# Optimization experiments

Measured on AMD Instinct MI355X. Metric: run time of the kernel, lower is better.

The kernel has to match this reference:

```python
import jax, jax.numpy as jnp
import numpy as np

NUM_PROJS = 7
BLOCK = 32

def _gray_perm(n):
    # unit-hamming-distance (Gray-code) permutation used by AngularLSH
    a = np.array([0, 1], dtype=np.int32)
    for s in range(2, n + 1):
        a = np.concatenate([a, a[::-1] + 2 ** (s - 1)])
    return a

PERM = jnp.asarray(_gray_perm(NUM_PROJS))
ENC = jnp.asarray(2 ** np.arange(NUM_PROJS), dtype=np.int32)  # [R]


def lsh_hash(x, proj_dir):
    # x: [B,H,S,D], proj_dir: [D,R] -> integer bucket ids [B,H,S]
    bits = (jnp.einsum('bhsd,dr->bhsr', x, proj_dir) > 0).astype(jnp.int32)
    code = (bits * ENC).sum(-1)
    return PERM[code]


def sdpa(q, k, v, mask):
    # q,k,v: [...,S,D]; mask: bool broadcastable to [...,Sq,Sk]
    scale = q.shape[-1] ** -0.5
    scores = jnp.einsum('...qd,...kd->...qk', q, k) * scale
    scores = jnp.where(mask, scores, -jnp.inf)
    return jnp.einsum('...qk,...kd->...qd', jax.nn.softmax(scores, axis=-1), v)


def setup_inputs() -> dict:
    key = jax.random.key(0)
    kq, kk, kv, kp = jax.random.split(key, 4)
    B, H, S, D = 2, 16, 2048, 128
    return {
        'q': jax.random.normal(kq, (B, H, S, D), dtype=jnp.float32),
        'k': jax.random.normal(kk, (B, H, S, D), dtype=jnp.float32),
        'v': jax.random.normal(kv, (B, H, S, D), dtype=jnp.float32),
        'proj_dir': jax.random.normal(kp, (D, NUM_PROJS), dtype=jnp.float32),
        'mask': jnp.ones((1, 1, 1, 1), dtype=bool),
    }


def reference(q, k, v, proj_dir, mask):
    B, H, S, D = q.shape
    # 1) LSH hash queries, stable sort along seq dim, reorder queries
    q_hash = lsh_hash(q, proj_dir)                                   # [B,H,S]
    sort_idx = jnp.argsort(q_hash, axis=2, stable=True)              # [B,H,S]
    q_hash_sorted = jnp.take_along_axis(q_hash, sort_idx, axis=2)
    q_sorted = jnp.take_along_axis(q, sort_idx[..., None], axis=2)   # [B,H,S,D]
    # 2) hash keys (unsorted), split into blocks of size BLOCK
    k_hash = lsh_hash(k, proj_dir)                                   # [B,H,S]
    k_hash_blk = k_hash.reshape(-1, 1, BLOCK)                        # [NB,1,32]
    q_hash_blk = q_hash_sorted.reshape(-1, 1, BLOCK)
    # 3) criticality: per-block count of matching hash ids; critical blocks get K zeroed
    criticality = (k_hash_blk == q_hash_blk).sum(-1).squeeze(-1)     # [NB]
    keep = (criticality <= 0).astype(q.dtype)                        # 0 where critical (matches torch loop)
    Qb = q_sorted.reshape(-1, 1, BLOCK, D)                           # [NB,1,32,D]
    Kb = k.reshape(-1, 1, BLOCK, D) * keep[:, None, None, None]
    Vb = v.reshape(-1, 1, BLOCK, D)
    # 4) dual SDPA: blocked critical attention + full dense attention
    out_critical = sdpa(Qb, Kb, Vb, mask).reshape(B, H, S, D)
    out_actual = sdpa(q, k, v, mask)                                 # [B,H,S,D]
    loss = jnp.mean((out_critical - out_actual) ** 2)
    return out_actual, loss
```

## Files before the change

kernel.cpp:

```cpp
#include <hip/hip_runtime.h>
#include <hip/hip_bf16.h>

#define SEQ 2048
#define DIM 128
#define NBH 32
#define NROWS (NBH*SEQ)
#define NBLK (NROWS/32)
#define SCALE 0.08838834764831845f
#define QSC (0.08838834764831845f * 1.4426950408889634f)

typedef __attribute__((ext_vector_type(8))) short short8;
typedef __attribute__((ext_vector_type(16))) float float16;

__device__ __forceinline__ unsigned short f2bf(float x) {
    union { float f; unsigned u; } v; v.f = x;
    unsigned r = v.u + 0x7fffu + ((v.u >> 16) & 1u);
    return (unsigned short)(r >> 16);
}
__device__ __forceinline__ unsigned pack_bf16(float a, float b) {
    float2 f; f.x = a; f.y = b;
    __hip_bfloat162 h = __float22bfloat162_rn(f);
    union { __hip_bfloat162 h2; unsigned u; } cv; cv.h2 = h; return cv.u;
}
__device__ __forceinline__ void gl_lds16(const void* g, void* l) {
    __builtin_amdgcn_global_load_lds((const __attribute__((address_space(1))) unsigned int*)g,
                                     (__attribute__((address_space(3))) unsigned int*)l, 16, 0, 0);
}

__global__ __launch_bounds__(256) void hash_kernel(const float* __restrict__ qg, const float* __restrict__ kg,
                            const float* __restrict__ proj,
                            int* __restrict__ qh, int* __restrict__ kh)
{
    const int gw   = (int)((blockIdx.x * blockDim.x + threadIdx.x) >> 6);
    const int lane = threadIdx.x & 63;
    const int sub  = lane >> 4;
    const int dl   = (lane & 15) * 8;
    const int r    = gw * 4 + sub;
    const float* src; int* dst; int row;
    if (r < NROWS) { src = qg; dst = qh; row = r; }
    else           { src = kg; dst = kh; row = r - NROWS; }

    const float* x = src + (size_t)row * DIM + dl;
    float xv[8];
    {
        float4 f0 = *(const float4*)x;
        float4 f1 = *(const float4*)(x + 4);
        xv[0]=f0.x; xv[1]=f0.y; xv[2]=f0.z; xv[3]=f0.w;
        xv[4]=f1.x; xv[5]=f1.y; xv[6]=f1.z; xv[7]=f1.w;
    }
    float pj[56];
    #pragma unroll
    for (int i = 0; i < 14; ++i)
        *(float4*)&pj[i*4] = *(const float4*)(proj + dl*7 + i*4);

    float a[7] = {0.f,0.f,0.f,0.f,0.f,0.f,0.f};
    #pragma unroll
    for (int d = 0; d < 8; ++d)
        #pragma unroll
        for (int p = 0; p < 7; ++p) a[p] = fmaf(xv[d], pj[d*7+p], a[p]);

    #pragma unroll
    for (int off = 1; off < 16; off <<= 1)
        #pragma unroll
        for (int p = 0; p < 7; ++p) a[p] += __shfl_xor(a[p], off, 64);

    if ((lane & 15) == 0) {
        int code = 0;
        if (a[0] > 0.f) code |= 1;  if (a[1] > 0.f) code |= 2;
        if (a[2] > 0.f) code |= 4;  if (a[3] > 0.f) code |= 8;
        if (a[4] > 0.f) code |= 16; if (a[5] > 0.f) code |= 32;
        if (a[6] > 0.f) code |= 64;
        dst[row] = code ^ (code >> 1);
    }
}

__global__ __launch_bounds__(256) void sort_kernel(const int* __restrict__ qh,
                                                   int* __restrict__ sidx, int* __restrict__ qhs)
{
    __shared__ unsigned short cnt[128][260];
    __shared__ int startv[128];
    const int bh = blockIdx.x;
    const int t  = threadIdx.x;
    const int base = bh*SEQ;

    for (int i = t; i < 128*260; i += 256) ((unsigned short*)cnt)[i] = 0;
    __syncthreads();

    int hv[8];
    {
        int4 a = *(const int4*)(qh + base + t*8);
        int4 b = *(const int4*)(qh + base + t*8 + 4);
        hv[0]=a.x; hv[1]=a.y; hv[2]=a.z; hv[3]=a.w;
        hv[4]=b.x; hv[5]=b.y; hv[6]=b.z; hv[7]=b.w;
    }
    #pragma unroll
    for (int i = 0; i < 8; ++i) cnt[hv[i]][t]++;
    __syncthreads();

    const int wv = t >> 6, l = t & 63;
    #pragma unroll 1
    for (int v = wv; v < 128; v += 4) {
        ushort4 cc = *(const ushort4*)&cnt[v][4*l];
        unsigned c0 = cc.x, c1 = cc.y, c2 = cc.z, c3 = cc.w;
        unsigned s01 = c0 + c1;
        unsigned s = s01 + c2 + c3;
        unsigned inc = s;
        #pragma unroll
        for (int off = 1; off < 64; off <<= 1) {
            unsigned o = __shfl_up(inc, off, 64);
            if (l >= off) inc += o;
        }
        unsigned ex = inc - s;
        ushort4 wb;
        wb.x = (unsigned short)ex;
        wb.y = (unsigned short)(ex + c0);
        wb.z = (unsigned short)(ex + s01);
        wb.w = (unsigned short)(ex + s01 + c2);
        *(ushort4*)&cnt[v][4*l] = wb;
        if (l == 63) cnt[v][256] = (unsigned short)inc;
    }
    __syncthreads();

    if (t < 64) {
        int a0 = cnt[2*t][256], a1 = cnt[2*t+1][256];
        int s2 = a0 + a1, inc = s2;
        #pragma unroll
        for (int off = 1; off < 64; off <<= 1) {
            int o = __shfl_up(inc, off, 64);
            if (t >= off) inc += o;
        }
        int ex = inc - s2;
        startv[2*t]   = ex;
        startv[2*t+1] = ex + a0;
    }
    __syncthreads();

    #pragma unroll
    for (int i = 0; i < 8; ++i) {
        const int v = hv[i];
        int prior = 0;
        #pragma unroll
        for (int j = 0; j < 8; ++j) if (j < i && hv[j] == v) ++prior;
        const int rank = startv[v] + (int)cnt[v][t] + prior;
        sidx[base + rank] = t*8 + i;
        qhs[base + rank]  = v;
    }
}

__global__ void crit_kernel(const int* __restrict__ kh, const int* __restrict__ qhs,
                            float* __restrict__ keepg)
{
    int nb = blockIdx.x * blockDim.x + threadIdx.x;
    if (nb >= NBLK) return;
    int c = 0;
    #pragma unroll
    for (int i = 0; i < 32; ++i) c += (kh[nb*32+i] == qhs[nb*32+i]) ? 1 : 0;
    keepg[nb] = (c == 0) ? 1.0f : 0.0f;
}

__global__ __launch_bounds__(256) void prep_kernel(const float* __restrict__ kg,
                                                   const float* __restrict__ vg,
                                                   unsigned short* __restrict__ kbf,
                                                   unsigned short* __restrict__ vtg)
{
    __shared__ unsigned short T[128][72];
    const int t  = threadIdx.x;
    const int h  = blockIdx.x >> 5;
    const int sl = blockIdx.x & 31;
    const size_t base = ((size_t)h*SEQ + sl*64) * DIM;

    #pragma unroll
    for (int i = 0; i < 8; ++i) {
        const float4 f = *(const float4*)(kg + base + ((size_t)i*256 + t)*4);
        uint2 pk; pk.x = pack_bf16(f.x, f.y); pk.y = pack_bf16(f.z, f.w);
        *(uint2*)(kbf + base + ((size_t)i*256 + t)*4) = pk;
    }

    const int kk = t & 63, seg = t >> 6;
    #pragma unroll
    for (int i = 0; i < 8; ++i) {
        float4 f = *(const float4*)(vg + base + (size_t)kk*DIM + seg*32 + i*4);
        T[seg*32 + i*4 + 0][kk] = f2bf(f.x);
        T[seg*32 + i*4 + 1][kk] = f2bf(f.y);
        T[seg*32 + i*4 + 2][kk] = f2bf(f.z);
        T[seg*32 + i*4 + 3][kk] = f2bf(f.w);
    }
    __syncthreads();
    const int r = t >> 1, hf = t & 1;
    unsigned short* dst = vtg + ((size_t)h*DIM + r)*SEQ + sl*64 + hf*32;
    #pragma unroll
    for (int i = 0; i < 4; ++i)
        *(short8*)(dst + i*8) = *(const short8*)&T[r][hf*32 + i*8];
}

__global__ __launch_bounds__(256, 2) void dense_attn_mfma(
    const unsigned short* __restrict__ kbf, const unsigned short* __restrict__ vtg,
    const float* __restrict__ qg, float* __restrict__ outg)
{
    __shared__ __align__(16) unsigned short KbF[2*8192];
    __shared__ __align__(16) unsigned short VbF[2*8192];

    const int t    = threadIdx.x;
    const int lane = t & 63;
    const int w    = t >> 6;
    const int q5   = lane >> 5;
    const int l31  = lane & 31;
    const int e    = l31 & 7;

    const int b    = blockIdx.x;
    const int slot = b >> 3;
    const int head = (b & 7) * 4 + (slot >> 4);
    const int qblk = slot & 15;

    const float* Qg = qg + ((size_t)head*SEQ + qblk*128 + w*32) * DIM;
    const unsigned short* Kh = kbf + (size_t)head*SEQ*DIM;
    const unsigned short* Vh = vtg + (size_t)head*DIM*SEQ;

    int koff[8], voff[4];
    #pragma unroll
    for (int ch = 0; ch < 8; ++ch) koff[ch] = l31*128 + (((2*ch + q5) ^ e) * 8);
    #pragma unroll
    for (int u = 0; u < 4; ++u)    voff[u]  = l31*64  + ((((u>>1)*4 + (u&1)*2 + q5) ^ e) * 8);

    const unsigned short* kgp[4]; unsigned short* kls[4];
    const unsigned short* vgp[4]; unsigned short* vls[4];
    #pragma unroll
    for (int i = 0; i < 4; ++i) {
        const int j = w*4 + i;
        const int r = j*4 + (lane >> 4);
        const int u = (lane & 15) ^ (r & 7);
        kgp[i] = Kh + r*DIM + u*8;
        kls[i] = KbF + j*512;
        const int d = j*8 + (lane >> 3);
        const int u2 = (lane & 7) ^ (d & 7);
        vgp[i] = Vh + (size_t)d*SEQ + u2*8;
        vls[i] = VbF + j*512;
    }

    union FR { unsigned u[4]; short8 s; };
    short8 Qf[8];
    #pragma unroll
    for (int ch = 0; ch < 8; ++ch) {
        const float* p = Qg + (size_t)l31*DIM + ch*16 + q5*8;
        float4 f0 = *(const float4*)p;
        float4 f1 = *(const float4*)(p + 4);
        FR fr;
        fr.u[0] = pack_bf16(f0.x*QSC, f0.y*QSC);
        fr.u[1] = pack_bf16(f0.z*QSC, f0.w*QSC);
        fr.u[2] = pack_bf16(f1.x*QSC, f1.y*QSC);
        fr.u[3] = pack_bf16(f1.z*QSC, f1.w*QSC);
        Qf[ch] = fr.s;
    }

    float16 o[4];
    #pragma unroll
    for (int mt = 0; mt < 4; ++mt)
        #pragma unroll
        for (int r = 0; r < 16; ++r) o[mt][r] = 0.f;
    float lsum = 0.f;

    auto stage = [&](const int buf) {
        #pragma unroll
        for (int i = 0; i < 4; ++i) gl_lds16(kgp[i], kls[i] + buf*8192);
        #pragma unroll
        for (int i = 0; i < 4; ++i) gl_lds16(vgp[i], vls[i] + buf*8192);
        #pragma unroll
        for (int i = 0; i < 4; ++i) { kgp[i] += 8192; vgp[i] += 64; }
    };

    auto body = [&](const int buf) {
        #pragma unroll
        for (int s = 0; s < 2; ++s) {
            float16 sv;
            #pragma unroll
            for (int r = 0; r < 16; ++r) sv[r] = 0.f;
            __builtin_amdgcn_s_setprio(1);
            #pragma unroll
            for (int ch = 0; ch < 8; ++ch) {
                short8 kf = *(const short8*)&KbF[buf*8192 + s*4096 + koff[ch]];
                sv = __builtin_amdgcn_mfma_f32_32x32x16_bf16(kf, Qf[ch], sv, 0, 0, 0);
            }
            __builtin_amdgcn_s_setprio(0);
            unsigned pk[8];
            #pragma unroll
            for (int rp = 0; rp < 8; ++rp) {
                float p0 = __builtin_amdgcn_exp2f(sv[2*rp]);
                float p1 = __builtin_amdgcn_exp2f(sv[2*rp+1]);
                lsum += p0 + p1;
                pk[rp] = pack_bf16(p0, p1);
            }
            unsigned e0 = __shfl_xor(q5 ? pk[0] : pk[2], 32, 64);
            unsigned e1 = __shfl_xor(q5 ? pk[1] : pk[3], 32, 64);
            unsigned e2 = __shfl_xor(q5 ? pk[4] : pk[6], 32, 64);
            unsigned e3 = __shfl_xor(q5 ? pk[5] : pk[7], 32, 64);
            FR c0, c1;
            if (q5 == 0) {
                c0.u[0]=pk[0]; c0.u[1]=pk[1]; c0.u[2]=e0;    c0.u[3]=e1;
                c1.u[0]=pk[4]; c1.u[1]=pk[5]; c1.u[2]=e2;    c1.u[3]=e3;
            } else {
                c0.u[0]=e0;    c0.u[1]=e1;    c0.u[2]=pk[2]; c0.u[3]=pk[3];
                c1.u[0]=e2;    c1.u[1]=e3;    c1.u[2]=pk[6]; c1.u[3]=pk[7];
            }
            __builtin_amdgcn_s_setprio(1);
            #pragma unroll
            for (int c = 0; c < 2; ++c) {
                short8 pf = c ? c1.s : c0.s;
                #pragma unroll
                for (int mt = 0; mt < 4; ++mt) {
                    short8 vf = *(const short8*)&VbF[buf*8192 + mt*2048 + voff[s*2 + c]];
                    o[mt] = __builtin_amdgcn_mfma_f32_32x32x16_bf16(vf, pf, o[mt], 0, 0, 0);
                }
            }
            __builtin_amdgcn_s_setprio(0);
        }
    };

    stage(0);
    stage(1);
    #pragma unroll 1
    for (int kt2 = 0; kt2 < 15; ++kt2) {
        asm volatile("s_waitcnt vmcnt(8)" ::: "memory");
        __builtin_amdgcn_s_barrier();
        body(0);
        asm volatile("s_waitcnt lgkmcnt(0)" ::: "memory");
        __builtin_amdgcn_s_barrier();
        stage(0);
        asm volatile("s_waitcnt vmcnt(8)" ::: "memory");
        __builtin_amdgcn_s_barrier();
        body(1);
        asm volatile("s_waitcnt lgkmcnt(0)" ::: "memory");
        __builtin_amdgcn_s_barrier();
        stage(1);
    }
    asm volatile("s_waitcnt vmcnt(8)" ::: "memory");
    __builtin_amdgcn_s_barrier();
    body(0);
    asm volatile("s_waitcnt vmcnt(0)" ::: "memory");
    __builtin_amdgcn_s_barrier();
    body(1);

    const float l = lsum + __shfl_xor(lsum, 32, 64);
    const float inv = 1.f / l;
    float* orow = outg + ((size_t)head*SEQ + qblk*128 + w*32 + l31) * DIM;
    #pragma unroll
    for (int mt = 0; mt < 4; ++mt)
        #pragma unroll
        for (int rg = 0; rg < 4; ++rg) {
            const int d0 = mt*32 + rg*8 + q5*4;
            float4 ov;
            ov.x = o[mt][rg*4+0]*inv; ov.y = o[mt][rg*4+1]*inv;
            ov.z = o[mt][rg*4+2]*inv; ov.w = o[mt][rg*4+3]*inv;
            *(float4*)(orow + d0) = ov;
        }
}

__global__ __launch_bounds__(256) void crit_attn(
    const unsigned short* __restrict__ kbf, const unsigned short* __restrict__ vtg,
    const float* __restrict__ qg, const int* __restrict__ sidx,
    const float* __restrict__ keepg, const float* __restrict__ outg, float* __restrict__ lossp)
{
    __shared__ float wsum[4];
    const int t    = threadIdx.x;
    const int lane = t & 63;
    const int w    = t >> 6;
    const int nb   = blockIdx.x * 4 + w;
    const int q5   = lane >> 5;
    const int l31  = lane & 31;
    const int bh   = nb >> 6;

    const float kp = keepg[nb];
    const int qrow = sidx[bh*SEQ + (nb & 63)*32 + l31];

    union FR { unsigned u[4]; short8 s; };
    short8 Qf[8];
    const float* Qg = qg + ((size_t)bh*SEQ + qrow) * DIM;
    #pragma unroll
    for (int ch = 0; ch < 8; ++ch) {
        const float* p = Qg + ch*16 + q5*8;
        float4 f0 = *(const float4*)p;
        float4 f1 = *(const float4*)(p + 4);
        FR fr;
        fr.u[0] = pack_bf16(f0.x*QSC, f0.y*QSC);
        fr.u[1] = pack_bf16(f0.z*QSC, f0.w*QSC);
        fr.u[2] = pack_bf16(f1.x*QSC, f1.y*QSC);
        fr.u[3] = pack_bf16(f1.z*QSC, f1.w*QSC);
        Qf[ch] = fr.s;
    }

    const unsigned short* Kb = kbf + (size_t)(nb*32) * DIM;
    float16 sv;
    #pragma unroll
    for (int r = 0; r < 16; ++r) sv[r] = 0.f;
    #pragma unroll
    for (int ch = 0; ch < 8; ++ch) {
        short8 kf = *(const short8*)(Kb + (size_t)l31*DIM + ch*16 + q5*8);
        sv = __builtin_amdgcn_mfma_f32_32x32x16_bf16(kf, Qf[ch], sv, 0, 0, 0);
    }

    float lsum = 0.f;
    unsigned pk[8];
    #pragma unroll
    for (int rp = 0; rp < 8; ++rp) {
        float p0 = __builtin_amdgcn_exp2f(sv[2*rp]   * kp);
        float p1 = __builtin_amdgcn_exp2f(sv[2*rp+1] * kp);
        lsum += p0 + p1;
        pk[rp] = pack_bf16(p0, p1);
    }
    unsigned e0 = __shfl_xor(q5 ? pk[0] : pk[2], 32, 64);
    unsigned e1 = __shfl_xor(q5 ? pk[1] : pk[3], 32, 64);
    unsigned e2 = __shfl_xor(q5 ? pk[4] : pk[6], 32, 64);
    unsigned e3 = __shfl_xor(q5 ? pk[5] : pk[7], 32, 64);
    FR c0, c1;
    if (q5 == 0) {
        c0.u[0]=pk[0]; c0.u[1]=pk[1]; c0.u[2]=e0;    c0.u[3]=e1;
        c1.u[0]=pk[4]; c1.u[1]=pk[5]; c1.u[2]=e2;    c1.u[3]=e3;
    } else {
        c0.u[0]=e0;    c0.u[1]=e1;    c0.u[2]=pk[2]; c0.u[3]=pk[3];
        c1.u[0]=e2;    c1.u[1]=e3;    c1.u[2]=pk[6]; c1.u[3]=pk[7];
    }
    const float ltot = lsum + __shfl_xor(lsum, 32, 64);

    const unsigned short* Vb = vtg + (size_t)bh*DIM*SEQ + (size_t)(nb & 63)*32;
    float16 o[4];
    #pragma unroll
    for (int mt = 0; mt < 4; ++mt)
        #pragma unroll
        for (int r = 0; r < 16; ++r) o[mt][r] = 0.f;
    #pragma unroll
    for (int c = 0; c < 2; ++c) {
        short8 pf = c ? c1.s : c0.s;
        #pragma unroll
        for (int mt = 0; mt < 4; ++mt) {
            short8 vf = *(const short8*)(Vb + (size_t)(mt*32 + l31)*SEQ + c*16 + q5*8);
            o[mt] = __builtin_amdgcn_mfma_f32_32x32x16_bf16(vf, pf, o[mt], 0, 0, 0);
        }
    }

    const float inv = 1.f / ltot;
    const float* oa_row = outg + (size_t)(nb*32 + l31) * DIM;
    float sq = 0.f;
    #pragma unroll
    for (int mt = 0; mt < 4; ++mt)
        #pragma unroll
        for (int rg = 0; rg < 4; ++rg) {
            const int d0 = mt*32 + rg*8 + q5*4;
            float4 oa = *(const float4*)(oa_row + d0);
            float dx = o[mt][rg*4+0]*inv - oa.x;
            float dy = o[mt][rg*4+1]*inv - oa.y;
            float dz = o[mt][rg*4+2]*inv - oa.z;
            float dw = o[mt][rg*4+3]*inv - oa.w;
            sq += dx*dx + dy*dy + dz*dz + dw*dw;
        }
    #pragma unroll
    for (int off = 32; off > 0; off >>= 1) sq += __shfl_down(sq, off, 64);
    if (lane == 0) wsum[w] = sq;
    __syncthreads();
    if (t == 0) atomicAdd(lossp, (wsum[0]+wsum[1]+wsum[2]+wsum[3]) * (1.0f/8388608.0f));
}

extern "C" void kernel_launch(void* const* d_in, const int* in_sizes, int n_in,
                              void* d_out, int out_size, void* d_ws, size_t ws_size,
                              hipStream_t stream)
{
    const float* q    = (const float*)d_in[0];
    const float* k    = (const float*)d_in[1];
    const float* v    = (const float*)d_in[2];
    const float* proj = (const float*)d_in[3];
    float* out   = (float*)d_out;
    float* lossp = out + (out_size - 1);

    int* qh   = (int*)d_ws;
    int* kh   = qh + NROWS;
    int* sidx = kh + NROWS;
    int* qhs  = sidx + NROWS;
    float* keepg = (float*)(qhs + NROWS);
    unsigned short* kbf = (unsigned short*)(keepg + NBLK);
    unsigned short* vtg = kbf + (size_t)NROWS*DIM;

    hipMemsetAsync(lossp, 0, sizeof(float), stream);
    prep_kernel<<<NBH*32, 256, 0, stream>>>(k, v, kbf, vtg);
    hash_kernel<<<(2*NROWS)/16, 256, 0, stream>>>(q, k, proj, qh, kh);
    sort_kernel<<<NBH, 256, 0, stream>>>(qh, sidx, qhs);
    crit_kernel<<<NBLK/256, 256, 0, stream>>>(kh, qhs, keepg);
    dense_attn_mfma<<<512, 256, 0, stream>>>(kbf, vtg, q, out);
    crit_attn<<<NBLK/4, 256, 0, stream>>>(kbf, vtg, q, sidx, keepg, out, lossp);
}
```

Before: 283.9 us.

## Fuse criticality into crit_attn, split QK MFMA chains, simplify dense pipeline

Removes the separate crit_kernel launch and computes each block's keep flag inside crit_attn using a wave ballot over the key and sorted query hashes. Both attention kernels now split the QK dot product into two independent MFMA accumulator chains, which shortens the dependency chain at the cost of extra registers. The dense kernel's loop is restructured into a single loop that prefetches only one tile ahead and waits on vmcnt(0) every iteration. That drops the earlier deeper prefetch, so less load latency may be hidden.

```diff
diff --git a/kernel.cpp b/kernel.cpp
--- a/kernel.cpp
+++ b/kernel.cpp
@@ -145,17 +145,6 @@
         sidx[base + rank] = t*8 + i;
         qhs[base + rank]  = v;
     }
-}
-
-__global__ void crit_kernel(const int* __restrict__ kh, const int* __restrict__ qhs,
-                            float* __restrict__ keepg)
-{
-    int nb = blockIdx.x * blockDim.x + threadIdx.x;
-    if (nb >= NBLK) return;
-    int c = 0;
-    #pragma unroll
-    for (int i = 0; i < 32; ++i) c += (kh[nb*32+i] == qhs[nb*32+i]) ? 1 : 0;
-    keepg[nb] = (c == 0) ? 1.0f : 0.0f;
 }
 
 __global__ __launch_bounds__(256) void prep_kernel(const float* __restrict__ kg,
@@ -237,6 +226,17 @@
         vls[i] = VbF + j*512;
     }
 
+    auto stage = [&](const int buf) {
+        #pragma unroll
+        for (int i = 0; i < 4; ++i) gl_lds16(kgp[i], kls[i] + buf*8192);
+        #pragma unroll
+        for (int i = 0; i < 4; ++i) gl_lds16(vgp[i], vls[i] + buf*8192);
+        #pragma unroll
+        for (int i = 0; i < 4; ++i) { kgp[i] += 8192; vgp[i] += 64; }
+    };
+
+    stage(0);
+
     union FR { unsigned u[4]; short8 s; };
     short8 Qf[8];
     #pragma unroll
@@ -257,36 +257,29 @@
     for (int mt = 0; mt < 4; ++mt)
         #pragma unroll
         for (int r = 0; r < 16; ++r) o[mt][r] = 0.f;
-    float lsum = 0.f;
-
-    auto stage = [&](const int buf) {
-        #pragma unroll
-        for (int i = 0; i < 4; ++i) gl_lds16(kgp[i], kls[i] + buf*8192);
-        #pragma unroll
-        for (int i = 0; i < 4; ++i) gl_lds16(vgp[i], vls[i] + buf*8192);
-        #pragma unroll
-        for (int i = 0; i < 4; ++i) { kgp[i] += 8192; vgp[i] += 64; }
-    };
+    float lsum0 = 0.f, lsum1 = 0.f;
 
     auto body = [&](const int buf) {
         #pragma unroll
         for (int s = 0; s < 2; ++s) {
-            float16 sv;
+            float16 sv, sw;
             #pragma unroll
-            for (int r = 0; r < 16; ++r) sv[r] = 0.f;
+            for (int r = 0; r < 16; ++r) { sv[r] = 0.f; sw[r] = 0.f; }
             __builtin_amdgcn_s_setprio(1);
             #pragma unroll
-            for (int ch = 0; ch < 8; ++ch) {
+            for (int ch = 0; ch < 4; ++ch) {
                 short8 kf = *(const short8*)&KbF[buf*8192 + s*4096 + koff[ch]];
                 sv = __builtin_amdgcn_mfma_f32_32x32x16_bf16(kf, Qf[ch], sv, 0, 0, 0);
+                short8 kg2 = *(const short8*)&KbF[buf*8192 + s*4096 + koff[ch+4]];
+                sw = __builtin_amdgcn_mfma_f32_32x32x16_bf16(kg2, Qf[ch+4], sw, 0, 0, 0);
             }
             __builtin_amdgcn_s_setprio(0);
             unsigned pk[8];
             #pragma unroll
             for (int rp = 0; rp < 8; ++rp) {
-                float p0 = __builtin_amdgcn_exp2f(sv[2*rp]);
-                float p1 = __builtin_amdgcn_exp2f(sv[2*rp+1]);
-                lsum += p0 + p1;
+                float p0 = __builtin_amdgcn_exp2f(sv[2*rp]   + sw[2*rp]);
+                float p1 = __builtin_amdgcn_exp2f(sv[2*rp+1] + sw[2*rp+1]);
+                lsum0 += p0; lsum1 += p1;
                 pk[rp] = pack_bf16(p0, p1);
             }
             unsigned e0 = __shfl_xor(q5 ? pk[0] : pk[2], 32, 64);
@@ -315,30 +308,15 @@
         }
     };
 
-    stage(0);
-    stage(1);
-    #pragma unroll 1
-    for (int kt2 = 0; kt2 < 15; ++kt2) {
-        asm volatile("s_waitcnt vmcnt(8)" ::: "memory");
+    #pragma unroll 2
+    for (int kt = 0; kt < 32; ++kt) {
+        asm volatile("s_waitcnt vmcnt(0) lgkmcnt(0)" ::: "memory");
         __builtin_amdgcn_s_barrier();
-        body(0);
-        asm volatile("s_waitcnt lgkmcnt(0)" ::: "memory");
-        __builtin_amdgcn_s_barrier();
-        stage(0);
-        asm volatile("s_waitcnt vmcnt(8)" ::: "memory");
-        __builtin_amdgcn_s_barrier();
-        body(1);
-        asm volatile("s_waitcnt lgkmcnt(0)" ::: "memory");
-        __builtin_amdgcn_s_barrier();
-        stage(1);
-    }
-    asm volatile("s_waitcnt vmcnt(8)" ::: "memory");
-    __builtin_amdgcn_s_barrier();
-    body(0);
-    asm volatile("s_waitcnt vmcnt(0)" ::: "memory");
-    __builtin_amdgcn_s_barrier();
-    body(1);
-
+        if (kt < 31) stage((kt & 1) ^ 1);
+        body(kt & 1);
+    }
+
+    const float lsum = lsum0 + lsum1;
     const float l = lsum + __shfl_xor(lsum, 32, 64);
     const float inv = 1.f / l;
     float* orow = outg + ((size_t)head*SEQ + qblk*128 + w*32 + l31) * DIM;
@@ -357,7 +335,8 @@
 __global__ __launch_bounds__(256) void crit_attn(
     const unsigned short* __restrict__ kbf, const unsigned short* __restrict__ vtg,
     const float* __restrict__ qg, const int* __restrict__ sidx,
-    const float* __restrict__ keepg, const float* __restrict__ outg, float* __restrict__ lossp)
+    const int* __restrict__ kh, const int* __restrict__ qhs,
+    const float* __restrict__ outg, float* __restrict__ lossp)
 {
     __shared__ float wsum[4];
     const int t    = threadIdx.x;
@@ -368,7 +347,11 @@
     const int l31  = lane & 31;
     const int bh   = nb >> 6;
 
-    const float kp = keepg[nb];
+    const int khv = kh[nb*32 + l31];
+    const int qhv = qhs[nb*32 + l31];
+    const unsigned long long mm = __ballot(khv == qhv);
+    const float kp = ((mm & 0xffffffffull) == 0ull) ? 1.0f : 0.0f;
+
     const int qrow = sidx[bh*SEQ + (nb & 63)*32 + l31];
 
     union FR { unsigned u[4]; short8 s; };
@@ -388,21 +371,23 @@
     }
 
     const unsigned short* Kb = kbf + (size_t)(nb*32) * DIM;
-    float16 sv;
-    #pragma unroll
-    for (int r = 0; r < 16; ++r) sv[r] = 0.f;
-    #pragma unroll
-    for (int ch = 0; ch < 8; ++ch) {
+    float16 sv, sw;
+    #pragma unroll
+    for (int r = 0; r < 16; ++r) { sv[r] = 0.f; sw[r] = 0.f; }
+    #pragma unroll
+    for (int ch = 0; ch < 4; ++ch) {
         short8 kf = *(const short8*)(Kb + (size_t)l31*DIM + ch*16 + q5*8);
         sv = __builtin_amdgcn_mfma_f32_32x32x16_bf16(kf, Qf[ch], sv, 0, 0, 0);
+        short8 kg2 = *(const short8*)(Kb + (size_t)l31*DIM + (ch+4)*16 + q5*8);
+        sw = __builtin_amdgcn_mfma_f32_32x32x16_bf16(kg2, Qf[ch+4], sw, 0, 0, 0);
     }
 
     float lsum = 0.f;
     unsigned pk[8];
     #pragma unroll
     for (int rp = 0; rp < 8; ++rp) {
-        float p0 = __builtin_amdgcn_exp2f(sv[2*rp]   * kp);
-        float p1 = __builtin_amdgcn_exp2f(sv[2*rp+1] * kp);
+        float p0 = __builtin_amdgcn_exp2f((sv[2*rp]   + sw[2*rp])   * kp);
+        float p1 = __builtin_amdgcn_exp2f((sv[2*rp+1] + sw[2*rp+1]) * kp);
         lsum += p0 + p1;
         pk[rp] = pack_bf16(p0, p1);
     }
@@ -473,15 +458,13 @@
     int* kh   = qh + NROWS;
     int* sidx = kh + NROWS;
     int* qhs  = sidx + NROWS;
-    float* keepg = (float*)(qhs + NROWS);
-    unsigned short* kbf = (unsigned short*)(keepg + NBLK);
+    unsigned short* kbf = (unsigned short*)(qhs + NROWS);
     unsigned short* vtg = kbf + (size_t)NROWS*DIM;
 
     hipMemsetAsync(lossp, 0, sizeof(float), stream);
     prep_kernel<<<NBH*32, 256, 0, stream>>>(k, v, kbf, vtg);
     hash_kernel<<<(2*NROWS)/16, 256, 0, stream>>>(q, k, proj, qh, kh);
     sort_kernel<<<NBH, 256, 0, stream>>>(qh, sidx, qhs);
-    crit_kernel<<<NBLK/256, 256, 0, stream>>>(kh, qhs, keepg);
     dense_attn_mfma<<<512, 256, 0, stream>>>(kbf, vtg, q, out);
-    crit_attn<<<NBLK/4, 256, 0, stream>>>(kbf, vtg, q, sidx, keepg, out, lossp);
-}
+    crit_attn<<<NBLK/4, 256, 0, stream>>>(kbf, vtg, q, sidx, kh, qhs, out, lossp);
+}
```

Measured after the change: 285.6 us. About the same (+0.6%).
